# Performance work log

Measured on AMD Instinct MI355X. Metric: run time of the kernel, lower is better.

## Reference

```python
import jax, jax.numpy as jnp
import numpy as np

B, L_DEC, V = 8, 256, 32000
L_SRC = 512
V_EXT = 32128


def setup_inputs() -> dict:
    key = jax.random.key(0)
    k1, k2, k3, k4 = jax.random.split(key, 4)
    dist_t = jax.random.uniform(k1, (B, L_DEC, V), dtype=jnp.float32)
    p_gen = jax.random.uniform(k2, (B, L_DEC, 1), dtype=jnp.float32)
    alph_t = jax.random.uniform(k3, (B, L_SRC, L_DEC), dtype=jnp.float32)
    batch_vocab = jnp.zeros((V_EXT,), dtype=jnp.float32)  # only shape[0] is used
    pointer = jax.random.randint(k4, (B, L_SRC), 0, V_EXT, dtype=jnp.int32)
    return {"dist_t": dist_t, "p_gen": p_gen, "alph_t": alph_t,
            "batch_vocab": batch_vocab, "pointer": pointer}


def reference(dist_t, p_gen, alph_t, batch_vocab, pointer):
    v_ext = batch_vocab.shape[0]
    nb, nl, ndim = dist_t.shape
    # p_gen * [vocab ; zeros padding up to extended vocab]
    prob_vocab = p_gen * jnp.pad(dist_t, ((0, 0), (0, 0), (0, v_ext - ndim)))
    # torch builds a dense one-hot [B, L_src, V_ext] and does bmm(alpha^T, one_hot).
    # Mathematically: copyp[b, t, v] = sum_{s : pointer[b,s]==v} alpha[b, s, t]
    # -> scatter-add of attention weights into pointed vocab slots.
    alpha_td = jnp.swapaxes(alph_t, 1, 2)  # [B, L_dec, L_src]

    def scatter_one(a_td, ptr):  # a_td: [L_dec, L_src], ptr: [L_src]
        return jnp.zeros((a_td.shape[0], v_ext), a_td.dtype).at[:, ptr].add(a_td)

    copyp = jax.vmap(scatter_one)(alpha_td, pointer)  # [B, L_dec, V_ext]
    proba = prob_vocab + (1.0 - p_gen) * copyp
    return proba
```

## Files before the change

kernel.cpp:

```cpp
#include <hip/hip_runtime.h>

#define B_     8
#define L_DEC_ 256
#define V_     32000
#define L_SRC_ 512
#define V_EXT_ 32128

#define V4_    (V_ / 4)
#define VE4_   (V_EXT_ / 4)

__global__ __launch_bounds__(256) void copynet_init(
    const float* __restrict__ dist,
    const float* __restrict__ p_gen,
    float* __restrict__ out)
{
    const int row  = blockIdx.y;
    const int col4 = blockIdx.x * blockDim.x + threadIdx.x;
    if (col4 >= VE4_) return;

    const float pg = p_gen[row];
    float4 r;
    if (col4 < V4_) {
        const float4 d = ((const float4*)dist)[(size_t)row * V4_ + col4];
        r.x = pg * d.x; r.y = pg * d.y; r.z = pg * d.z; r.w = pg * d.w;
    } else {
        r = make_float4(0.f, 0.f, 0.f, 0.f);
    }
    ((float4*)out)[(size_t)row * VE4_ + col4] = r;
}

__global__ __launch_bounds__(256) void copynet_scatter(
    const float* __restrict__ alph,
    const float* __restrict__ p_gen,
    const int*   __restrict__ pointer,
    float* __restrict__ out)
{
    const int bs = blockIdx.x;
    const int b  = bs >> 9;
    const int t  = threadIdx.x;

    const int   v    = pointer[bs];
    const float a    = alph[(size_t)bs * L_DEC_ + t];
    const float coef = 1.0f - p_gen[b * L_DEC_ + t];

    atomicAdd(out + (size_t)(b * L_DEC_ + t) * V_EXT_ + v, coef * a);
}

extern "C" void kernel_launch(void* const* d_in, const int* in_sizes, int n_in,
                              void* d_out, int out_size, void* d_ws, size_t ws_size,
                              hipStream_t stream)
{
    const float* dist    = (const float*)d_in[0];
    const float* p_gen   = (const float*)d_in[1];
    const float* alph    = (const float*)d_in[2];
    const int*   pointer = (const int*)d_in[4];
    float* out = (float*)d_out;

    dim3 grid1((VE4_ + 255) / 256, B_ * L_DEC_);
    copynet_init<<<grid1, 256, 0, stream>>>(dist, p_gen, out);

    copynet_scatter<<<B_ * L_SRC_, 256, 0, stream>>>(alph, p_gen, pointer, out);
}
```

Measured before the change: 487.4 us.

## Fuse scaling and pointer scatter into one per-row kernel with LDS accumulation

Replaces the separate init and global-atomic scatter kernels with one kernel per output row. Each block builds the copy distribution for half the extended vocabulary at a time in shared memory using LDS atomics, then writes p_gen*dist plus the copy term with float4 stores. This removes the second launch and the scattered global atomics into the output. In exchange, each block reads alpha with a strided gather (stride L_DEC) and uses about 64KB of LDS, which may reduce occupancy.

After: 439.0 us. 9.9% less time.

```diff
diff --git a/kernel.cpp b/kernel.cpp
--- a/kernel.cpp
+++ b/kernel.cpp
@@ -9,41 +9,60 @@
 #define V4_    (V_ / 4)
 #define VE4_   (V_EXT_ / 4)
 
-__global__ __launch_bounds__(256) void copynet_init(
+#define HALF_  16064
+#define HALF4_ (HALF_ / 4)
+
+__global__ __launch_bounds__(512) void copynet_fused(
     const float* __restrict__ dist,
     const float* __restrict__ p_gen,
-    float* __restrict__ out)
-{
-    const int row  = blockIdx.y;
-    const int col4 = blockIdx.x * blockDim.x + threadIdx.x;
-    if (col4 >= VE4_) return;
-
-    const float pg = p_gen[row];
-    float4 r;
-    if (col4 < V4_) {
-        const float4 d = ((const float4*)dist)[(size_t)row * V4_ + col4];
-        r.x = pg * d.x; r.y = pg * d.y; r.z = pg * d.z; r.w = pg * d.w;
-    } else {
-        r = make_float4(0.f, 0.f, 0.f, 0.f);
-    }
-    ((float4*)out)[(size_t)row * VE4_ + col4] = r;
-}
-
-__global__ __launch_bounds__(256) void copynet_scatter(
     const float* __restrict__ alph,
-    const float* __restrict__ p_gen,
     const int*   __restrict__ pointer,
     float* __restrict__ out)
 {
-    const int bs = blockIdx.x;
-    const int b  = bs >> 9;
-    const int t  = threadIdx.x;
+    __shared__ float cp[HALF_];
 
-    const int   v    = pointer[bs];
-    const float a    = alph[(size_t)bs * L_DEC_ + t];
-    const float coef = 1.0f - p_gen[b * L_DEC_ + t];
+    const int row = blockIdx.x;
+    const int b   = row >> 8;
+    const int t   = row & (L_DEC_ - 1);
+    const int tid = threadIdx.x;
 
-    atomicAdd(out + (size_t)(b * L_DEC_ + t) * V_EXT_ + v, coef * a);
+    const float pg   = p_gen[row];
+    const float coef = 1.0f - pg;
+
+    const int   sIdx = b * L_SRC_ + tid;
+    const int   v    = pointer[sIdx];
+    const float val  = coef * alph[(size_t)sIdx * L_DEC_ + t];
+
+    const float4* dist4 = (const float4*)(dist + (size_t)row * V_);
+    float4*       out4  = (float4*)(out + (size_t)row * V_EXT_);
+    float4*       cp4   = (float4*)cp;
+
+#pragma unroll
+    for (int h = 0; h < 2; ++h) {
+        for (int i = tid; i < HALF4_; i += 512)
+            cp4[i] = make_float4(0.f, 0.f, 0.f, 0.f);
+        __syncthreads();
+
+        const int lo = h * HALF_;
+        if ((unsigned)(v - lo) < (unsigned)HALF_)
+            atomicAdd(&cp[v - lo], val);
+        __syncthreads();
+
+        const int base4 = h * HALF4_;
+        for (int i = tid; i < HALF4_; i += 512) {
+            const int g4 = base4 + i;
+            float4 r = cp4[i];
+            if (g4 < V4_) {
+                const float4 d = dist4[g4];
+                r.x = fmaf(pg, d.x, r.x);
+                r.y = fmaf(pg, d.y, r.y);
+                r.z = fmaf(pg, d.z, r.z);
+                r.w = fmaf(pg, d.w, r.w);
+            }
+            out4[g4] = r;
+        }
+        __syncthreads();
+    }
 }
 
 extern "C" void kernel_launch(void* const* d_in, const int* in_sizes, int n_in,
@@ -56,8 +75,5 @@
     const int*   pointer = (const int*)d_in[4];
     float* out = (float*)d_out;
 
-    dim3 grid1((VE4_ + 255) / 256, B_ * L_DEC_);
-    copynet_init<<<grid1, 256, 0, stream>>>(dist, p_gen, out);
-
-    copynet_scatter<<<B_ * L_SRC_, 256, 0, stream>>>(alph, p_gen, pointer, out);
+    copynet_fused<<<B_ * L_DEC_, 512, 0, stream>>>(dist, p_gen, alph, pointer, out);
 }
```
